# Optimization experiments

Hardware: AMD Instinct MI355X
Metric: run time of the kernel (lower is better)

The kernel has to match this reference:

```python
import jax, jax.numpy as jnp
import numpy as np

EPS_LN = 1e-5
EPS_NORM = 1e-12


def _layernorm(h, g, b):
    mu = jnp.mean(h, axis=-1, keepdims=True)
    var = jnp.mean((h - mu) ** 2, axis=-1, keepdims=True)
    return (h - mu) * jax.lax.rsqrt(var + EPS_LN) * g + b


def _l2norm(h):
    n = jnp.linalg.norm(h, axis=-1, keepdims=True)
    return h / jnp.maximum(n, EPS_NORM)


def setup_inputs() -> dict:
    key = jax.random.key(0)
    ks = jax.random.split(key, 6)
    B, S, D = 8, 4096, 1024
    A, C, dc = 16, 8, 64      # n_anchors, n_comp, d_comp
    apc = A // C              # anchors per compartment = 2
    x = jax.random.normal(ks[0], (B, S, D), jnp.float32)
    anchors = jax.random.normal(ks[1], (A, D), jnp.float32)  # normalized inside forward
    ln_g = jnp.ones((D,), jnp.float32)
    ln_b = jnp.zeros((D,), jnp.float32)
    W1 = jax.random.normal(ks[2], (C, apc, 2 * dc), jnp.float32) / np.sqrt(apc)
    b1 = jnp.zeros((C, 2 * dc), jnp.float32)
    W2 = jax.random.normal(ks[3], (C, 2 * dc, dc), jnp.float32) / np.sqrt(2 * dc)
    b2 = jnp.zeros((C, dc), jnp.float32)
    cg = jnp.ones((C, dc), jnp.float32)
    cb = jnp.zeros((C, dc), jnp.float32)
    Wp = jax.random.normal(ks[4], (C * dc, D), jnp.float32) / np.sqrt(C * dc)
    bp = jnp.zeros((D,), jnp.float32)
    gate = jnp.full((D,), -3.0, jnp.float32)  # gate_init = -3.0
    return dict(x=x, anchors=anchors, ln_g=ln_g, ln_b=ln_b, W1=W1, b1=b1,
                W2=W2, b2=b2, cg=cg, cb=cb, Wp=Wp, bp=bp, gate=gate)


def reference(x, anchors, ln_g, ln_b, W1, b1, W2, b2, cg, cb, Wp, bp, gate):
    B, S, D = x.shape
    C, apc, _ = W1.shape
    dc = W2.shape[-1]
    # LayerNorm then L2-normalize each token
    h = _l2norm(_layernorm(x.reshape(B * S, D), ln_g, ln_b))  # (N, D)
    a = _l2norm(anchors)                                      # (A, D)
    tri = 1.0 - h @ a.T                                       # (N, A)
    # asgn = arange(A) % C -> comp k reads columns [k, k+C, ...]
    g = tri.reshape(-1, apc, C)                               # g[:, j, k] = tri[:, j*C + k]
    u = jnp.einsum('nak,kae->nke', g, W1) + b1                # (N, C, 2*dc)
    u = jnp.square(jnp.maximum(u, 0.0))                       # squared ReLU
    y = jnp.einsum('nke,ked->nkd', u, W2) + b2                # (N, C, dc)
    y = _layernorm(y, cg, cb)                                 # per-comp LayerNorm over dc
    y = y.reshape(-1, C * dc)                                 # concat comps in order
    update = (y @ Wp + bp).reshape(B, S, D)
    return x + jax.nn.sigmoid(gate) * update
```

## Files before the change

### kernel.cpp

```cpp
#include <hip/hip_runtime.h>
#include <hip/hip_bf16.h>

#define DIM 1024
#define NANCH 16
#define NCOMP 8
#define DC 64
#define DC2 128
#define EPS_LN 1e-5f
#define EPS_NORM 1e-12f

typedef __bf16 bf16x8 __attribute__((ext_vector_type(8)));
typedef float f32x4 __attribute__((ext_vector_type(4)));

template <int CTRL>
__device__ __forceinline__ float rr_add(float v) {
  return v + __int_as_float(__builtin_amdgcn_update_dpp(
                 0, __float_as_int(v), CTRL, 0xF, 0xF, true));
}
__device__ __forceinline__ float rowsum16(float v) {
  v = rr_add<0x121>(v);
  v = rr_add<0x122>(v);
  v = rr_add<0x124>(v);
  v = rr_add<0x128>(v);
  return v;
}
__device__ __forceinline__ float wavesum64(float v) {
  v = rowsum16(v);
  v += __shfl_xor(v, 16);
  v += __shfl_xor(v, 32);
  return v;
}

__device__ __forceinline__ void gload16(const void* g, void* l) {
  __builtin_amdgcn_global_load_lds(
      (const __attribute__((address_space(1))) unsigned int*)g,
      (__attribute__((address_space(3))) unsigned int*)l, 16, 0, 0);
}

__global__ __launch_bounds__(256) void kprepall(
    const float* __restrict__ anchors, const float* __restrict__ Wp,
    const float* __restrict__ W2, __hip_bfloat16* __restrict__ WpT,
    __hip_bfloat16* __restrict__ W2B, __hip_bfloat16* __restrict__ AnB) {
  __shared__ float smem[64 * 65 + 16];
  int b = blockIdx.x, t = threadIdx.x;

  if (b < 16) {
    int a = b, lane = t & 63, wid = t >> 6;
    float v[4]; float ss = 0.f;
#pragma unroll
    for (int i = 0; i < 4; i++) {
      v[i] = anchors[a * DIM + t + 256 * i];
      ss += v[i] * v[i];
    }
    for (int off = 32; off; off >>= 1) ss += __shfl_down(ss, off);
    if (lane == 0) smem[4160 + wid] = ss;
    __syncthreads();
    float inv = 1.f / fmaxf(sqrtf(smem[4160] + smem[4161] + smem[4162] + smem[4163]),
                            EPS_NORM);
#pragma unroll
    for (int i = 0; i < 4; i++) smem[t + 256 * i] = v[i] * inv;
    __syncthreads();
#pragma unroll
    for (int q = 0; q < 4; q++) {
      int idx = t * 4 + q;
      int ks = idx >> 5, hi = (idx >> 3) & 3, j = idx & 7;
      AnB[ks * 512 + (hi * 16 + a) * 8 + j] = __float2bfloat16(smem[idx]);
    }
  } else if (b < 144) {
    int bidx = b - 16, bj = bidx & 15, bk = bidx >> 4;
    int tx = t & 63, ty = t >> 6;
#pragma unroll
    for (int i = 0; i < 16; i++) {
      int r = ty + 4 * i;
      smem[r * 65 + tx] = Wp[(size_t)(bk * 64 + r) * DIM + bj * 64 + tx];
    }
    __syncthreads();
#pragma unroll
    for (int i = 0; i < 16; i++) {
      int r = ty + 4 * i;
      WpT[(size_t)(bj * 64 + r) * 512 + bk * 64 + tx] =
          __float2bfloat16(smem[tx * 65 + r]);
    }
  } else {
    int id = (b - 144) * 256 + t;
    int j = id & 7, lane = (id >> 3) & 63, ks = (id >> 9) & 3,
        nt = (id >> 11) & 3, k = id >> 13;
    int e = ks * 32 + (lane >> 4) * 8 + j;
    int n = nt * 16 + (lane & 15);
    W2B[id] = __float2bfloat16(W2[k * (DC2 * DC) + e * DC + n]);
  }
}

#define LDA_H 1032
__global__ __launch_bounds__(256, 7) void kt1(
    const float* __restrict__ x, const __hip_bfloat16* __restrict__ AnB,
    const float* __restrict__ ln_g, const float* __restrict__ ln_b,
    float* __restrict__ triG) {
  int t = threadIdx.x;
  int lane = t & 63, w = t >> 6;
  int l15 = lane & 15, quad = lane >> 4;
  int n0 = blockIdx.x * 8;

  __shared__ __hip_bfloat16 hs[8 * LDA_H];
  __shared__ float part[4 * 32 * 4];

  float gv[16], bv[16];
#pragma unroll
  for (int i = 0; i < 4; i++) {
    f32x4 g4 = *(const f32x4*)(&ln_g[i * 256 + lane * 4]);
    f32x4 b4 = *(const f32x4*)(&ln_b[i * 256 + lane * 4]);
#pragma unroll
    for (int j = 0; j < 4; j++) { gv[i * 4 + j] = g4[j]; bv[i * 4 + j] = b4[j]; }
  }
#pragma unroll
  for (int it = 0; it < 2; it++) {
    int tok = w * 2 + it;
    const float* xr = x + (size_t)(n0 + tok) * DIM;
    float xv[16], s = 0.f, s2 = 0.f;
#pragma unroll
    for (int i = 0; i < 4; i++) {
      f32x4 v4 = *(const f32x4*)(&xr[i * 256 + lane * 4]);
#pragma unroll
      for (int j = 0; j < 4; j++) {
        float v = v4[j];
        xv[i * 4 + j] = v; s += v; s2 += v * v;
      }
    }
    s = wavesum64(s);
    s2 = wavesum64(s2);
    float mu = s * (1.f / DIM);
    float rstd = rsqrtf(s2 * (1.f / DIM) - mu * mu + EPS_LN);
    float ss = 0.f;
#pragma unroll
    for (int i = 0; i < 16; i++) {
      float h = (xv[i] - mu) * rstd * gv[i] + bv[i];
      xv[i] = h; ss += h * h;
    }
    ss = wavesum64(ss);
    float inv = 1.f / fmaxf(sqrtf(ss), EPS_NORM);
#pragma unroll
    for (int i = 0; i < 4; i++) {
      union { uint2 u; __hip_bfloat16 h[4]; } pk;
#pragma unroll
      for (int j = 0; j < 4; j++) pk.h[j] = __float2bfloat16(xv[i * 4 + j] * inv);
      *(uint2*)(&hs[tok * LDA_H + i * 256 + lane * 4]) = pk.u;
    }
  }
  __syncthreads();

  {
    f32x4 tacc = {0.f, 0.f, 0.f, 0.f};
    int ar = l15 & 7;
#pragma unroll
    for (int ks = w * 8; ks < w * 8 + 8; ks++) {
      bf16x8 afr = *(const bf16x8*)(&hs[ar * LDA_H + ks * 32 + quad * 8]);
      bf16x8 bfr = *(const bf16x8*)(&AnB[ks * 512 + lane * 8]);
      tacc = __builtin_amdgcn_mfma_f32_16x16x32_bf16(afr, bfr, tacc, 0, 0, 0);
    }
    if (quad < 2) *(f32x4*)(&part[(w * 32 + (lane & 31)) * 4]) = tacc;
  }
  __syncthreads();
  if (t < 128) {
    int ln = t & 31, rg = t >> 5;
    float v = part[(0 * 32 + ln) * 4 + rg] + part[(1 * 32 + ln) * 4 + rg] +
              part[(2 * 32 + ln) * 4 + rg] + part[(3 * 32 + ln) * 4 + rg];
    int m = (ln >> 4) * 4 + rg, a = ln & 15;
    triG[(size_t)(n0 + m) * 16 + a] = 1.f - v;
  }
}

__global__ __launch_bounds__(256, 7) void kt2(
    const float* __restrict__ triG, const float* __restrict__ W1,
    const float* __restrict__ b1, const __hip_bfloat16* __restrict__ W2B,
    const float* __restrict__ b2, const float* __restrict__ cg,
    const float* __restrict__ cb, __hip_bfloat16* __restrict__ yout) {
  int t = threadIdx.x;
  int lane = t & 63, w = t >> 6;
  int l15 = lane & 15, quad = lane >> 4;
  int n0 = blockIdx.x * 8;

  __shared__ __hip_bfloat16 us[8 * LDA_H];
  __shared__ float tri_s[8 * 16];

  if (t < 128) tri_s[t] = triG[(size_t)n0 * 16 + t];
  __syncthreads();

  {
    int k = t >> 5;
    int e0 = (t * 4) & 127;
    f32x4 w1a = *(const f32x4*)(&W1[k * 256 + e0]);
    f32x4 w1b = *(const f32x4*)(&W1[k * 256 + 128 + e0]);
    f32x4 b1v = *(const f32x4*)(&b1[k * 128 + e0]);
#pragma unroll
    for (int tok = 0; tok < 8; tok++) {
      float t0 = tri_s[tok * 16 + k], t1 = tri_s[tok * 16 + 8 + k];
      union { unsigned long long u; __hip_bfloat16 h[4]; } pk;
#pragma unroll
      for (int j = 0; j < 4; j++) {
        float uu = t0 * w1a[j] + t1 * w1b[j] + b1v[j];
        uu = fmaxf(uu, 0.f);
        pk.h[j] = __float2bfloat16(uu * uu);
      }
      *(unsigned long long*)(&us[tok * LDA_H + t * 4]) = pk.u;
    }
  }
  __syncthreads();

#pragma unroll
  for (int kc = 0; kc < 2; kc++) {
    int k = w * 2 + kc;
    int ar = l15 & 7;
    bf16x8 afr[4];
#pragma unroll
    for (int ks = 0; ks < 4; ks++)
      afr[ks] = *(const bf16x8*)(&us[ar * LDA_H + k * 128 + ks * 32 + quad * 8]);
    f32x4 acc[4] = {{0,0,0,0},{0,0,0,0},{0,0,0,0},{0,0,0,0}};
#pragma unroll
    for (int nt = 0; nt < 4; nt++) {
#pragma unroll
      for (int ks = 0; ks < 4; ks++) {
        bf16x8 bfr = *(const bf16x8*)(&W2B[(size_t)(((k * 4 + nt) * 4 + ks)) * 512 + lane * 8]);
        acc[nt] = __builtin_amdgcn_mfma_f32_16x16x32_bf16(afr[ks], bfr, acc[nt], 0, 0, 0);
      }
    }
    float vals[4][4], s1[4] = {0,0,0,0}, s2[4] = {0,0,0,0};
#pragma unroll
    for (int nt = 0; nt < 4; nt++) {
      float b2v = b2[k * 64 + nt * 16 + l15];
#pragma unroll
      for (int r = 0; r < 4; r++) {
        float v = acc[nt][r] + b2v;
        vals[nt][r] = v; s1[r] += v; s2[r] += v * v;
      }
    }
#pragma unroll
    for (int r = 0; r < 4; r++) {
      s1[r] = rowsum16(s1[r]);
      s2[r] = rowsum16(s2[r]);
    }
#pragma unroll
    for (int r = 0; r < 4; r++) {
      float mu = s1[r] * (1.f / DC);
      float rs = rsqrtf(s2[r] * (1.f / DC) - mu * mu + EPS_LN);
      int tokrow = quad * 4 + r;
      if (tokrow < 8) {
#pragma unroll
        for (int nt = 0; nt < 4; nt++) {
          int d = nt * 16 + l15;
          float yn = (vals[nt][r] - mu) * rs * cg[k * 64 + d] + cb[k * 64 + d];
          yout[(size_t)(n0 + tokrow) * 512 + k * 64 + d] = __float2bfloat16(yn);
        }
      }
    }
  }
}

__global__ __launch_bounds__(256, 4) void kgemm(
    const __hip_bfloat16* __restrict__ Y, const __hip_bfloat16* __restrict__ WpT,
    const float* __restrict__ x, const float* __restrict__ bp,
    const float* __restrict__ gate, float* __restrict__ out) {
  __shared__ alignas(16) __hip_bfloat16 As[128 * 64];
  __shared__ alignas(16) __hip_bfloat16 Bs[128 * 64];
  int t = threadIdx.x, lane = t & 63, wid = t >> 6;
  int bm = blockIdx.x, bj = blockIdx.y;
  int wm = (wid >> 1) * 64, wj = (wid & 1) * 64;
  int l15 = lane & 15, quad = lane >> 4;

  f32x4 acc[4][4] = {};

  int srow[4], scol[4];
#pragma unroll
  for (int it = 0; it < 4; it++) {
    int byteo = it * 4096 + t * 16;
    int row = byteo >> 7, colb = byteo & 127;
    srow[it] = row;
    scol[it] = (colb ^ ((row & 7) << 4)) >> 1;
  }

  for (int kt = 0; kt < 8; kt++) {
    int k0 = kt * 64;
#pragma unroll
    for (int it = 0; it < 4; it++) {
      gload16(Y + (size_t)(bm * 128 + srow[it]) * 512 + k0 + scol[it],
              As + (it * 4096 + t * 16) / 2);
      gload16(WpT + (size_t)(bj * 128 + srow[it]) * 512 + k0 + scol[it],
              Bs + (it * 4096 + t * 16) / 2);
    }
    __syncthreads();
#pragma unroll
    for (int kk = 0; kk < 64; kk += 32) {
      bf16x8 af[4], bfr[4];
#pragma unroll
      for (int i = 0; i < 4; i++) {
        int ra = wm + i * 16 + l15, rb = wj + i * 16 + l15;
        int cb2 = (kk + quad * 8) * 2;
        af[i]  = *(const bf16x8*)((const char*)As + ra * 128 + (cb2 ^ ((ra & 7) << 4)));
        bfr[i] = *(const bf16x8*)((const char*)Bs + rb * 128 + (cb2 ^ ((rb & 7) << 4)));
      }
#pragma unroll
      for (int i = 0; i < 4; i++)
#pragma unroll
        for (int j = 0; j < 4; j++)
          acc[i][j] = __builtin_amdgcn_mfma_f32_16x16x32_bf16(af[i], bfr[j], acc[i][j], 0, 0, 0);
    }
    __syncthreads();
  }

  float sg[4], bpv[4];
#pragma unroll
  for (int j = 0; j < 4; j++) {
    int gc = bj * 128 + wj + j * 16 + l15;
    sg[j] = 1.f / (1.f + expf(-gate[gc]));
    bpv[j] = bp[gc];
  }
#pragma unroll
  for (int i = 0; i < 4; i++) {
#pragma unroll
    for (int j = 0; j < 4; j++) {
      int gc = bj * 128 + wj + j * 16 + l15;
#pragma unroll
      for (int r = 0; r < 4; r++) {
        int gr = bm * 128 + wm + i * 16 + quad * 4 + r;
        size_t idx = (size_t)gr * DIM + gc;
        out[idx] = x[idx] + sg[j] * (acc[i][j][r] + bpv[j]);
      }
    }
  }
}

extern "C" void kernel_launch(void* const* d_in, const int* in_sizes, int n_in,
                              void* d_out, int out_size, void* d_ws, size_t ws_size,
                              hipStream_t stream) {
  const float* x       = (const float*)d_in[0];
  const float* anchors = (const float*)d_in[1];
  const float* ln_g    = (const float*)d_in[2];
  const float* ln_b    = (const float*)d_in[3];
  const float* W1      = (const float*)d_in[4];
  const float* b1      = (const float*)d_in[5];
  const float* W2      = (const float*)d_in[6];
  const float* b2      = (const float*)d_in[7];
  const float* cg      = (const float*)d_in[8];
  const float* cb      = (const float*)d_in[9];
  const float* Wp      = (const float*)d_in[10];
  const float* bp      = (const float*)d_in[11];
  const float* gate    = (const float*)d_in[12];

  int N = in_sizes[0] / DIM;

  char* w = (char*)d_ws;
  size_t off = 0;
  __hip_bfloat16* WpT = (__hip_bfloat16*)(w + off);  off += 1 << 20;
  __hip_bfloat16* W2B = (__hip_bfloat16*)(w + off);  off += 128 << 10;
  __hip_bfloat16* AnB = (__hip_bfloat16*)(w + off);  off += 32 << 10;
  float* triG         = (float*)(w + off);           off += (size_t)N * 16 * 4;
  __hip_bfloat16* Yb  = (__hip_bfloat16*)(w + off);

  kprepall<<<400, 256, 0, stream>>>(anchors, Wp, W2, WpT, W2B, AnB);
  kt1<<<N / 8, 256, 0, stream>>>(x, AnB, ln_g, ln_b, triG);
  kt2<<<N / 8, 256, 0, stream>>>(triG, W1, b1, W2B, b2, cg, cb, Yb);
  kgemm<<<dim3(N / 128, DIM / 128), 256, 0, stream>>>(Yb, WpT, x, bp, gate,
                                                      (float*)d_out);
}
```

Measured before the change: 358.4 us.

## Make kt1 persistent over four token groups with register prefetch of x

kt1 now processes four 8-token groups per block instead of one, launching a quarter as many blocks. While it computes LayerNorm, L2 normalization and the anchor MFMA for the current group, it prefetches the next group's x rows into registers to hide global load latency. The cost is higher register pressure, a lower occupancy target (launch bounds 4 instead of 7), fewer blocks to spread across CUs, and an extra barrier per group.

```diff
diff --git a/kernel.cpp b/kernel.cpp
--- a/kernel.cpp
+++ b/kernel.cpp
@@ -92,14 +92,14 @@
 }
 
 #define LDA_H 1032
-__global__ __launch_bounds__(256, 7) void kt1(
+#define KT1_GPB 4
+__global__ __launch_bounds__(256, 4) void kt1(
     const float* __restrict__ x, const __hip_bfloat16* __restrict__ AnB,
     const float* __restrict__ ln_g, const float* __restrict__ ln_b,
     float* __restrict__ triG) {
   int t = threadIdx.x;
   int lane = t & 63, w = t >> 6;
   int l15 = lane & 15, quad = lane >> 4;
-  int n0 = blockIdx.x * 8;
 
   __shared__ __hip_bfloat16 hs[8 * LDA_H];
   __shared__ float part[4 * 32 * 4];
@@ -112,60 +112,88 @@
 #pragma unroll
     for (int j = 0; j < 4; j++) { gv[i * 4 + j] = g4[j]; bv[i * 4 + j] = b4[j]; }
   }
-#pragma unroll
-  for (int it = 0; it < 2; it++) {
-    int tok = w * 2 + it;
-    const float* xr = x + (size_t)(n0 + tok) * DIM;
-    float xv[16], s = 0.f, s2 = 0.f;
+
+  int g0 = blockIdx.x * KT1_GPB;
+
+  f32x4 nx0[4], nx1[4];
+  {
+    const float* xr0 = x + (size_t)(g0 * 8 + w * 2) * DIM;
 #pragma unroll
     for (int i = 0; i < 4; i++) {
-      f32x4 v4 = *(const f32x4*)(&xr[i * 256 + lane * 4]);
-#pragma unroll
-      for (int j = 0; j < 4; j++) {
-        float v = v4[j];
-        xv[i * 4 + j] = v; s += v; s2 += v * v;
-      }
-    }
-    s = wavesum64(s);
-    s2 = wavesum64(s2);
-    float mu = s * (1.f / DIM);
-    float rstd = rsqrtf(s2 * (1.f / DIM) - mu * mu + EPS_LN);
-    float ss = 0.f;
-#pragma unroll
-    for (int i = 0; i < 16; i++) {
-      float h = (xv[i] - mu) * rstd * gv[i] + bv[i];
-      xv[i] = h; ss += h * h;
-    }
-    ss = wavesum64(ss);
-    float inv = 1.f / fmaxf(sqrtf(ss), EPS_NORM);
-#pragma unroll
-    for (int i = 0; i < 4; i++) {
-      union { uint2 u; __hip_bfloat16 h[4]; } pk;
-#pragma unroll
-      for (int j = 0; j < 4; j++) pk.h[j] = __float2bfloat16(xv[i * 4 + j] * inv);
-      *(uint2*)(&hs[tok * LDA_H + i * 256 + lane * 4]) = pk.u;
-    }
-  }
-  __syncthreads();
-
-  {
-    f32x4 tacc = {0.f, 0.f, 0.f, 0.f};
-    int ar = l15 & 7;
-#pragma unroll
-    for (int ks = w * 8; ks < w * 8 + 8; ks++) {
-      bf16x8 afr = *(const bf16x8*)(&hs[ar * LDA_H + ks * 32 + quad * 8]);
-      bf16x8 bfr = *(const bf16x8*)(&AnB[ks * 512 + lane * 8]);
-      tacc = __builtin_amdgcn_mfma_f32_16x16x32_bf16(afr, bfr, tacc, 0, 0, 0);
-    }
-    if (quad < 2) *(f32x4*)(&part[(w * 32 + (lane & 31)) * 4]) = tacc;
-  }
-  __syncthreads();
-  if (t < 128) {
-    int ln = t & 31, rg = t >> 5;
-    float v = part[(0 * 32 + ln) * 4 + rg] + part[(1 * 32 + ln) * 4 + rg] +
-              part[(2 * 32 + ln) * 4 + rg] + part[(3 * 32 + ln) * 4 + rg];
-    int m = (ln >> 4) * 4 + rg, a = ln & 15;
-    triG[(size_t)(n0 + m) * 16 + a] = 1.f - v;
+      nx0[i] = *(const f32x4*)(&xr0[i * 256 + lane * 4]);
+      nx1[i] = *(const f32x4*)(&xr0[DIM + i * 256 + lane * 4]);
+    }
+  }
+
+  for (int g = g0; g < g0 + KT1_GPB; ++g) {
+    int n0 = g * 8;
+    f32x4 cx0[4], cx1[4];
+#pragma unroll
+    for (int i = 0; i < 4; i++) { cx0[i] = nx0[i]; cx1[i] = nx1[i]; }
+    if (g + 1 < g0 + KT1_GPB) {
+      const float* xr1 = x + (size_t)((g + 1) * 8 + w * 2) * DIM;
+#pragma unroll
+      for (int i = 0; i < 4; i++) {
+        nx0[i] = *(const f32x4*)(&xr1[i * 256 + lane * 4]);
+        nx1[i] = *(const f32x4*)(&xr1[DIM + i * 256 + lane * 4]);
+      }
+    }
+
+#pragma unroll
+    for (int it = 0; it < 2; it++) {
+      int tok = w * 2 + it;
+      float xv[16], s = 0.f, s2 = 0.f;
+#pragma unroll
+      for (int i = 0; i < 4; i++) {
+        f32x4 v4 = (it == 0) ? cx0[i] : cx1[i];
+#pragma unroll
+        for (int j = 0; j < 4; j++) {
+          float v = v4[j];
+          xv[i * 4 + j] = v; s += v; s2 += v * v;
+        }
+      }
+      s = wavesum64(s);
+      s2 = wavesum64(s2);
+      float mu = s * (1.f / DIM);
+      float rstd = rsqrtf(s2 * (1.f / DIM) - mu * mu + EPS_LN);
+      float ss = 0.f;
+#pragma unroll
+      for (int i = 0; i < 16; i++) {
+        float h = (xv[i] - mu) * rstd * gv[i] + bv[i];
+        xv[i] = h; ss += h * h;
+      }
+      ss = wavesum64(ss);
+      float inv = 1.f / fmaxf(sqrtf(ss), EPS_NORM);
+#pragma unroll
+      for (int i = 0; i < 4; i++) {
+        union { uint2 u; __hip_bfloat16 h[4]; } pk;
+#pragma unroll
+        for (int j = 0; j < 4; j++) pk.h[j] = __float2bfloat16(xv[i * 4 + j] * inv);
+        *(uint2*)(&hs[tok * LDA_H + i * 256 + lane * 4]) = pk.u;
+      }
+    }
+    __syncthreads();
+
+    {
+      f32x4 tacc = {0.f, 0.f, 0.f, 0.f};
+      int ar = l15 & 7;
+#pragma unroll
+      for (int ks = w * 8; ks < w * 8 + 8; ks++) {
+        bf16x8 afr = *(const bf16x8*)(&hs[ar * LDA_H + ks * 32 + quad * 8]);
+        bf16x8 bfr = *(const bf16x8*)(&AnB[ks * 512 + lane * 8]);
+        tacc = __builtin_amdgcn_mfma_f32_16x16x32_bf16(afr, bfr, tacc, 0, 0, 0);
+      }
+      if (quad < 2) *(f32x4*)(&part[(w * 32 + (lane & 31)) * 4]) = tacc;
+    }
+    __syncthreads();
+    if (t < 128) {
+      int ln = t & 31, rg = t >> 5;
+      float v = part[(0 * 32 + ln) * 4 + rg] + part[(1 * 32 + ln) * 4 + rg] +
+                part[(2 * 32 + ln) * 4 + rg] + part[(3 * 32 + ln) * 4 + rg];
+      int m = (ln >> 4) * 4 + rg, a = ln & 15;
+      triG[(size_t)(n0 + m) * 16 + a] = 1.f - v;
+    }
+    __syncthreads();
   }
 }
 
@@ -356,7 +384,7 @@
   __hip_bfloat16* Yb  = (__hip_bfloat16*)(w + off);
 
   kprepall<<<400, 256, 0, stream>>>(anchors, Wp, W2, WpT, W2B, AnB);
-  kt1<<<N / 8, 256, 0, stream>>>(x, AnB, ln_g, ln_b, triG);
+  kt1<<<(N / 8) / KT1_GPB, 256, 0, stream>>>(x, AnB, ln_g, ln_b, triG);
   kt2<<<N / 8, 256, 0, stream>>>(triG, W1, b1, W2B, b2, cg, cb, Yb);
   kgemm<<<dim3(N / 128, DIM / 128), 256, 0, stream>>>(Yb, WpT, x, bp, gate,
                                                       (float*)d_out);
```

Result: slower. 379.5 us (+5.9%).
